# Kernel tuning notes

Hardware: AMD Instinct MI355X
Metric: run time of the kernel (lower is better)

Reference implementation:

```python
import jax, jax.numpy as jnp
import numpy as np
import math

WP, WF = 10, 10      # past/future window
EPS = 1e-8           # torch cosine_similarity eps
CLIP = 1.0 - 1e-6    # keep arccos (and its grad) finite
MAXN = 110           # hard-coded alpha width in the module


def setup_inputs() -> dict:
    key = jax.random.key(0)
    k1, k2, k3, k4, k5, k6 = jax.random.split(key, 6)
    B, L, G, N, D = 32, 110, 512, 40, 300
    node_features = jax.random.normal(k1, (B, L, G), jnp.float32)
    knowledge = jax.random.normal(k2, (B, L, N, D), jnp.float32)
    anew = jax.random.uniform(k3, (B, L, N), jnp.float32)
    var_sem = 2.0 / (G + G)
    var_con = 2.0 / (D + D)
    weight_sem = jax.random.normal(k4, (G, G), jnp.float32) * var_sem
    weight_con = jax.random.normal(k5, (D, D), jnp.float32) * var_con
    text_len = jax.random.randint(k6, (B,), 55, L + 1, jnp.int32)
    return dict(node_features=node_features, knowledge=knowledge, anew=anew,
                weight_sem=weight_sem, weight_con=weight_con, text_len=text_len)


def reference(node_features, knowledge, anew, weight_sem, weight_con, text_len):
    B, L, G = node_features.shape
    N = knowledge.shape[2]
    dt = node_features.dtype

    # window + validity mask, replaces per-(i,j) python slicing: [B, j, k]
    j = jnp.arange(L)[:, None]
    k = jnp.arange(L)[None, :]
    cur = text_len[:, None, None]
    mask = (k >= j - WP) & (k <= j + WF)
    mask = mask[None] & (k[None, :, :] <= cur - 1) & (j[None, :, :] < cur)
    fmask = mask.astype(dt)

    # ---- semantic branch: score = 1 - acos(cos_sim(f_j, W_sem f_k))/pi, windowed softmax
    att_sem = jnp.einsum('st,blt->bls', weight_sem, node_features)      # [B,L,G]
    num = jnp.einsum('bjg,bkg->bjk', node_features, att_sem)
    nf = jnp.maximum(jnp.linalg.norm(node_features, axis=-1), EPS)      # [B,L]
    na = jnp.maximum(jnp.linalg.norm(att_sem, axis=-1), EPS)            # [B,L]
    cos = num / (nf[:, :, None] * na[:, None, :])
    score = 1.0 - jnp.arccos(jnp.clip(cos, -CLIP, CLIP)) / math.pi
    neg = jnp.finfo(dt).min
    s = jnp.where(mask, score, neg)
    s = s - jnp.max(s, axis=-1, keepdims=True)
    e = jnp.exp(s) * fmask
    alphas_sem = e / jnp.maximum(jnp.sum(e, axis=-1, keepdims=True), EPS)  # [B,L,L]

    # ---- affinity transform of anew: v -> (||[v, v/2] - [0.5, 0]|| - 0.06467)/0.607468
    anew_aff = (jnp.sqrt((anew - 0.5) ** 2 + (0.5 * anew) ** 2) - 0.06467) / 0.607468

    # ---- contextual branch: windowed sum_n |cos_sim(aff_feat_{k,n}, knowledge_{j,n})|
    att_con = jnp.einsum('blns,st->blnt', knowledge, weight_con)        # [B,L,N,D]
    aff_feat = att_con * anew_aff[..., None]                            # [B,L,N,D]
    num_c = jnp.einsum('bknd,bjnd->bjkn', aff_feat, knowledge)          # [B,j,k,N]
    n_f = jnp.maximum(jnp.linalg.norm(aff_feat, axis=-1), EPS)          # [B,k,N]
    n_k = jnp.maximum(jnp.linalg.norm(knowledge, axis=-1), EPS)         # [B,j,N]
    cos_c = num_c / (n_f[:, None, :, :] * n_k[:, :, None, :])
    alphas_con = 10.0 * jnp.sum(jnp.abs(cos_c), axis=-1) * fmask        # [B,j,k]

    out = 0.5 * alphas_sem + 0.5 * alphas_con                           # [B,L,L]
    if L < MAXN:  # module hard-codes width 110
        out = jnp.pad(out, ((0, 0), (0, 0), (0, MAXN - L)))
    return out
```

## Files before the change

kernel.cpp:

```cpp
#include <hip/hip_runtime.h>
#include <hip/hip_bf16.h>
#include <math.h>

constexpr int Bb   = 32;
constexpr int Ls   = 110;
constexpr int Gs   = 512;
constexpr int Ns   = 40;
constexpr int Ds   = 300;
constexpr int WPc  = 10;
constexpr int WFc  = 10;
constexpr int MAXNc = 110;
constexpr float EPSf  = 1e-8f;
constexpr float CLIPf = 1.0f - 1e-6f;
constexpr int BL = Bb * Ls;
constexpr int Mrows = BL * Ns;
constexpr int BPITCH = 328;
constexpr int KST = 320;
constexpr int RGRP = Mrows / 256;

typedef __attribute__((ext_vector_type(8))) short short8_t;
typedef __attribute__((ext_vector_type(4))) short short4_t;
typedef __attribute__((ext_vector_type(4))) float floatx4;

__device__ __forceinline__ unsigned short bf16r(float f) {
  unsigned u = __float_as_uint(f);
  u += 0x7fffu + ((u >> 16) & 1u);
  return (unsigned short)(u >> 16);
}

__device__ __forceinline__ unsigned pkbf(float lo, float hi) {
  unsigned a = __float_as_uint(lo), b = __float_as_uint(hi);
  a += 0x7fffu + ((a >> 16) & 1u);
  b += 0x7fffu + ((b >> 16) & 1u);
  return (a >> 16) | (b & 0xffff0000u);
}

__device__ __forceinline__ short8_t cvt8(const float4 v0, const float4 v1) {
  union { short8_t s; unsigned u[4]; } p;
  p.u[0] = pkbf(v0.x, v0.y);
  p.u[1] = pkbf(v0.z, v0.w);
  p.u[2] = pkbf(v1.x, v1.y);
  p.u[3] = pkbf(v1.z, v1.w);
  return p.s;
}

__global__ __launch_bounds__(256) void transpose_wsem(const float* __restrict__ w,
                                                      float* __restrict__ wt) {
  __shared__ float tile[32][33];
  const int bx = blockIdx.x * 32;
  const int by = blockIdx.y * 32;
  const int tx = threadIdx.x;
  const int ty = threadIdx.y;
#pragma unroll
  for (int r = ty; r < 32; r += 8)
    tile[r][tx] = w[(by + r) * Gs + (bx + tx)];
  __syncthreads();
#pragma unroll
  for (int r = ty; r < 32; r += 8)
    wt[(bx + r) * Gs + (by + tx)] = tile[tx][r];
}

__global__ __launch_bounds__(256) void wct_prep(const float* __restrict__ wc,
                                                short* __restrict__ wct) {
  __shared__ float tile[32][33];
  const int t0 = blockIdx.x * 32;
  const int s0 = blockIdx.y * 32;
  const int tx = threadIdx.x, ty = threadIdx.y;
#pragma unroll
  for (int r = ty; r < 32; r += 8) {
    const int s = s0 + r, t = t0 + tx;
    tile[r][tx] = (s < Ds && t < Ds) ? wc[s * Ds + t] : 0.f;
  }
  __syncthreads();
#pragma unroll
  for (int r = ty; r < 32; r += 8) {
    const int t = t0 + r, s = s0 + tx;
    wct[t * KST + s] = (short)bf16r(tile[tx][r]);
  }
}

__global__ __launch_bounds__(256) void kn_prep(const float* __restrict__ kn,
                                               unsigned short* __restrict__ knb,
                                               float* __restrict__ kninv) {
  const int wid = (blockIdx.x * 256 + threadIdx.x) >> 6;
  const int lane = threadIdx.x & 63;
  const int nwaves = gridDim.x * 4;
  for (int row = wid; row < Mrows; row += nwaves) {
    const float* __restrict__ src = kn + (size_t)row * Ds;
    float4 v0 = make_float4(0.f, 0.f, 0.f, 0.f);
    float4 v1 = v0;
    const int d0 = lane * 8;
    if (lane < 37) {
      v0 = *reinterpret_cast<const float4*>(src + d0);
      v1 = *reinterpret_cast<const float4*>(src + d0 + 4);
    } else if (lane == 37) {
      v0 = *reinterpret_cast<const float4*>(src + d0);
    }
    float ss = v0.x * v0.x + v0.y * v0.y + v0.z * v0.z + v0.w * v0.w +
               v1.x * v1.x + v1.y * v1.y + v1.z * v1.z + v1.w * v1.w;
#pragma unroll
    for (int off = 32; off > 0; off >>= 1) ss += __shfl_xor(ss, off);
    if (lane < 40)
      *reinterpret_cast<short8_t*>(knb + (size_t)row * KST + d0) = cvt8(v0, v1);
    if (lane == 0) kninv[row] = 1.0f / fmaxf(sqrtf(ss), EPSf);
  }
}

__global__ __launch_bounds__(512) void sem_gemm(const float* __restrict__ nf,
                                                const float* __restrict__ wt,
                                                float* __restrict__ att_sem,
                                                float* __restrict__ na_arr) {
  const int bl0 = blockIdx.x * 8;
  const int s = threadIdx.x;
  const float* __restrict__ x0 = nf + (size_t)bl0 * Gs;
  float acc[8];
#pragma unroll
  for (int r = 0; r < 8; ++r) acc[r] = 0.f;
#pragma unroll 4
  for (int t = 0; t < Gs; ++t) {
    const float wv = wt[t * Gs + s];
#pragma unroll
    for (int r = 0; r < 8; ++r) acc[r] = fmaf(wv, x0[r * Gs + t], acc[r]);
  }
#pragma unroll
  for (int r = 0; r < 8; ++r) att_sem[(size_t)(bl0 + r) * Gs + s] = acc[r];

  __shared__ float partial[8][8];
  const int wave = s >> 6, lane = s & 63;
#pragma unroll
  for (int r = 0; r < 8; ++r) {
    float v = acc[r] * acc[r];
#pragma unroll
    for (int off = 32; off > 0; off >>= 1) v += __shfl_xor(v, off);
    if (lane == 0) partial[r][wave] = v;
  }
  __syncthreads();
  if (s < 8) {
    float sum = 0.f;
#pragma unroll
    for (int w2 = 0; w2 < 8; ++w2) sum += partial[s][w2];
    na_arr[bl0 + s] = fmaxf(sqrtf(sum), EPSf);
  }
}

__global__ __launch_bounds__(256) void sem_attn(const float* __restrict__ nf,
                                                const float* __restrict__ att_sem,
                                                const float* __restrict__ na_arr,
                                                const int* __restrict__ tlen,
                                                float* __restrict__ out) {
  const int blk = blockIdx.x;
  const int b = blk / Ls, j = blk % Ls;
  const int len = tlen[b];
  float* __restrict__ orow = out + (size_t)(b * Ls + j) * MAXNc;
  if (j >= len) {
    for (int k = threadIdx.x; k < MAXNc; k += 256) orow[k] = 0.f;
    return;
  }
  const int k0 = max(j - WPc, 0);
  const int k1 = min(j + WFc, len - 1);
  const int nk = k1 - k0 + 1;

  __shared__ float xs[Gs];
  __shared__ float sc[21];
  __shared__ float red[4];

  const float* __restrict__ x = nf + (size_t)(b * Ls + j) * Gs;
  float ss = 0.f;
  for (int t = threadIdx.x; t < Gs; t += 256) {
    const float v = x[t];
    xs[t] = v;
    ss += v * v;
  }
  const int wave = threadIdx.x >> 6, lane = threadIdx.x & 63;
#pragma unroll
  for (int off = 32; off > 0; off >>= 1) ss += __shfl_xor(ss, off);
  if (lane == 0) red[wave] = ss;
  __syncthreads();
  const float nfn = fmaxf(sqrtf(red[0] + red[1] + red[2] + red[3]), EPSf);

  for (int i = wave; i < nk; i += 4) {
    const int k = k0 + i;
    const float* __restrict__ as = att_sem + (size_t)(b * Ls + k) * Gs;
    float d = 0.f;
#pragma unroll
    for (int t = lane; t < Gs; t += 64) d = fmaf(xs[t], as[t], d);
#pragma unroll
    for (int off = 32; off > 0; off >>= 1) d += __shfl_xor(d, off);
    if (lane == 0) {
      float cs = d / (nfn * na_arr[b * Ls + k]);
      cs = fminf(fmaxf(cs, -CLIPf), CLIPf);
      sc[i] = 1.0f - acosf(cs) * (float)(1.0 / M_PI);
    }
  }
  __syncthreads();
  if (threadIdx.x == 0) {
    float m = -1e30f;
    for (int i = 0; i < nk; ++i) m = fmaxf(m, sc[i]);
    red[0] = m;
  }
  __syncthreads();
  const float m = red[0];
  if ((int)threadIdx.x < nk) sc[threadIdx.x] = expf(sc[threadIdx.x] - m);
  __syncthreads();
  if (threadIdx.x == 0) {
    float s = 0.f;
    for (int i = 0; i < nk; ++i) s += sc[i];
    red[1] = 1.0f / fmaxf(s, EPSf);
  }
  __syncthreads();
  const float inv = red[1];
  for (int k = threadIdx.x; k < MAXNc; k += 256) {
    float v = 0.f;
    if (k >= k0 && k <= k1) v = 0.5f * sc[k - k0] * inv;
    orow[k] = v;
  }
}

__global__ __launch_bounds__(256, 3) void con_gemm_mfma(const unsigned short* __restrict__ knb,
                                                        const short* __restrict__ wct,
                                                        const int* __restrict__ tlen,
                                                        unsigned short* __restrict__ ybar,
                                                        float* __restrict__ rowss) {
  const int lin = blockIdx.x;
  const int xcd = lin & 7, slot = lin >> 3;
  const int m = slot & 3;
  const int g = xcd + 8 * (slot >> 2);
  if (g >= RGRP) return;
  const int rowbase = g * 256;
  const int n0 = m * 80;

  __shared__ short Bl[80 * BPITCH];
  const int tid = threadIdx.x;
  for (int s = tid; s < 80 * 40; s += 256) {
    const int nl = s / 40, sl = s % 40;
    *reinterpret_cast<short8_t*>(&Bl[nl * BPITCH + sl * 8]) =
        *reinterpret_cast<const short8_t*>(wct + (n0 + nl) * KST + sl * 8);
  }
  __syncthreads();

  const int wave = tid >> 6, lane = tid & 63;
  const int quad = lane >> 4, l16 = lane & 15;
  const int wrow = rowbase + wave * 64;

  {
    bool any = false;
    for (int bl = wrow / Ns; bl <= (wrow + 63) / Ns; ++bl)
      any |= (bl % Ls) < tlen[bl / Ls];
    if (!any) return;
  }

  const unsigned short* arow[4];
#pragma unroll
  for (int tt = 0; tt < 4; ++tt)
    arow[tt] = knb + (size_t)(wrow + tt * 16 + l16) * KST + quad * 8;

  floatx4 acc[4][5];
#pragma unroll
  for (int tt = 0; tt < 4; ++tt)
#pragma unroll
    for (int i = 0; i < 5; ++i) acc[tt][i] = (floatx4){0.f, 0.f, 0.f, 0.f};

  short8_t A[3][4];
#pragma unroll
  for (int tt = 0; tt < 4; ++tt) {
    A[0][tt] = *reinterpret_cast<const short8_t*>(arow[tt]);
    A[1][tt] = *reinterpret_cast<const short8_t*>(arow[tt] + 32);
  }

#pragma unroll
  for (int c = 0; c < 10; ++c) {
    if (c < 8) {
#pragma unroll
      for (int tt = 0; tt < 4; ++tt)
        A[(c + 2) % 3][tt] =
            *reinterpret_cast<const short8_t*>(arow[tt] + (c + 2) * 32);
    }
#pragma unroll
    for (int i = 0; i < 5; ++i) {
      const short8_t bfrag = *reinterpret_cast<const short8_t*>(
          &Bl[(i * 16 + l16) * BPITCH + c * 32 + quad * 8]);
#pragma unroll
      for (int tt = 0; tt < 4; ++tt)
        acc[tt][i] = __builtin_amdgcn_mfma_f32_16x16x32_bf16(A[c % 3][tt], bfrag,
                                                             acc[tt][i], 0, 0, 0);
    }
  }

#pragma unroll
  for (int tt = 0; tt < 4; ++tt) {
    const int row0 = wrow + tt * 16;
    const int blA = row0 / Ns, blB = (row0 + 15) / Ns;
    const bool alive = ((blA % Ls) < tlen[blA / Ls]) | ((blB % Ls) < tlen[blB / Ls]);
    if (!alive) continue;
#pragma unroll
    for (int r = 0; r < 4; ++r) {
      float p = 0.f;
#pragma unroll
      for (int i = 0; i < 5; ++i) p = fmaf(acc[tt][i][r], acc[tt][i][r], p);
      p += __shfl_xor(p, 1);
      p += __shfl_xor(p, 2);
      p += __shfl_xor(p, 4);
      p += __shfl_xor(p, 8);
      if (l16 == 0) atomicAdd(&rowss[row0 + quad * 4 + r], p);
    }
#pragma unroll
    for (int i = 0; i < 5; ++i) {
      const int col = n0 + i * 16 + l16;
#pragma unroll
      for (int r = 0; r < 4; ++r)
        ybar[(size_t)(row0 + quad * 4 + r) * KST + col] = bf16r(acc[tt][i][r]);
    }
  }
}

__global__ __launch_bounds__(512) void con_attn_mfma(const unsigned short* __restrict__ knb,
                                                     const unsigned short* __restrict__ ybar,
                                                     const float* __restrict__ rowss,
                                                     const float* __restrict__ kninv,
                                                     const float* __restrict__ anew,
                                                     const int* __restrict__ tlen,
                                                     float* __restrict__ out) {
  const int b = blockIdx.x / 7;
  const int jt = blockIdx.x % 7;
  const int j0 = jt * 16;
  const int len = tlen[b];
  if (j0 >= len) return;
  const int kbase = min(max(j0 - WPc, 0), Ls - 48);

  const int tid = threadIdx.x;
  const int wave = tid >> 6, lane = tid & 63;
  const int quad = lane >> 4, l16 = lane & 15;

  __shared__ float red[8][768];

  const int jj = min(j0 + l16, Ls - 1);
  const size_t blj = (size_t)(b * Ls + jj);

  float outacc[3][4];
#pragma unroll
  for (int t = 0; t < 3; ++t)
#pragma unroll
    for (int r = 0; r < 4; ++r) outacc[t][r] = 0.f;

  const unsigned short* yrow[3];
  int krow_m[3];
#pragma unroll
  for (int t = 0; t < 3; ++t) {
    const int k = kbase + t * 16 + l16;
    yrow[t] = ybar + (size_t)(b * Ls + k) * Ns * KST;
    krow_m[t] = (b * Ls + k) * Ns;
  }

  for (int ni = 0; ni < 5; ++ni) {
    const int n = wave + ni * 8;
    const unsigned short* __restrict__ arow =
        knb + ((blj * Ns + n) * (size_t)KST) + quad * 8;

    float w_t[3];
#pragma unroll
    for (int t = 0; t < 3; ++t) {
      const int mm = krow_m[t] + n;
      const float a = anew[mm];
      const float ssqk = rowss[mm];
      const float aff = (sqrtf((a - 0.5f) * (a - 0.5f) + 0.25f * a * a) - 0.06467f) *
                        (1.0f / 0.607468f);
      w_t[t] = aff / fmaxf(aff * sqrtf(ssqk), EPSf);
    }
    const float kinv = kninv[blj * Ns + n];

    floatx4 S[3];
#pragma unroll
    for (int t = 0; t < 3; ++t) S[t] = (floatx4){0.f, 0.f, 0.f, 0.f};

#pragma unroll
    for (int c = 0; c < 10; ++c) {
      const short8_t afrag = *reinterpret_cast<const short8_t*>(arow + c * 32);
#pragma unroll
      for (int t = 0; t < 3; ++t) {
        const short8_t bfrag = *reinterpret_cast<const short8_t*>(
            yrow[t] + (size_t)n * KST + c * 32 + quad * 8);
        S[t] = __builtin_amdgcn_mfma_f32_16x16x32_bf16(afrag, bfrag, S[t], 0, 0, 0);
      }
    }

#pragma unroll
    for (int r = 0; r < 4; ++r) {
      const float kv = __shfl(kinv, quad * 4 + r);
#pragma unroll
      for (int t = 0; t < 3; ++t)
        outacc[t][r] = fmaf(kv * w_t[t], fabsf(S[t][r]), outacc[t][r]);
    }
  }

#pragma unroll
  for (int t = 0; t < 3; ++t)
#pragma unroll
    for (int r = 0; r < 4; ++r)
      red[wave][(quad * 4 + r) * 48 + t * 16 + l16] = outacc[t][r];
  __syncthreads();

  for (int idx = tid; idx < 768; idx += 512) {
    float s = 0.f;
#pragma unroll
    for (int w = 0; w < 8; ++w) s += red[w][idx];
    const int j = j0 + idx / 48;
    const int k = kbase + idx % 48;
    if (j < len && k < len && k >= j - WPc && k <= j + WFc)
      out[(size_t)(b * Ls + j) * MAXNc + k] += 5.0f * s;
  }
}

extern "C" void kernel_launch(void* const* d_in, const int* in_sizes, int n_in,
                              void* d_out, int out_size, void* d_ws, size_t ws_size,
                              hipStream_t stream) {
  const float* nf   = (const float*)d_in[0];
  const float* kn   = (const float*)d_in[1];
  const float* anew = (const float*)d_in[2];
  const float* wsem = (const float*)d_in[3];
  const float* wcon = (const float*)d_in[4];
  const int*   tlen = (const int*)d_in[5];
  float* out = (float*)d_out;

  float* att_sem = (float*)d_ws;
  float* na_arr  = att_sem + (size_t)BL * Gs;
  float* wt      = na_arr + BL;
  short* wct     = (short*)(wt + (size_t)Gs * Gs);
  float* rowss   = (float*)(wct + KST * KST);
  float* kninv   = rowss + Mrows;
  unsigned short* knb  = (unsigned short*)(kninv + Mrows);
  unsigned short* ybar = knb + (size_t)Mrows * KST;

  hipMemsetAsync(rowss, 0, (size_t)Mrows * sizeof(float), stream);
  transpose_wsem<<<dim3(16, 16), dim3(32, 8), 0, stream>>>(wsem, wt);
  wct_prep<<<dim3(10, 10), dim3(32, 8), 0, stream>>>(wcon, wct);
  kn_prep<<<2048, 256, 0, stream>>>(kn, knb, kninv);
  sem_gemm<<<BL / 8, 512, 0, stream>>>(nf, wt, att_sem, na_arr);
  sem_attn<<<BL, 256, 0, stream>>>(nf, att_sem, na_arr, tlen, out);
  con_gemm_mfma<<<2208, 256, 0, stream>>>(knb, wct, tlen, ybar, rowss);
  con_attn_mfma<<<Bb * 7, 512, 0, stream>>>(knb, ybar, rowss, kninv, anew, tlen, out);
}
```

Baseline: 482.7 us.

## Fuse knowledge bf16 conversion and norm into GEMM and attention kernels

Result: slower. 783.8 us (+62.4%).

```diff
diff --git a/kernel.cpp b/kernel.cpp
--- a/kernel.cpp
+++ b/kernel.cpp
@@ -79,33 +79,6 @@
   }
 }
 
-__global__ __launch_bounds__(256) void kn_prep(const float* __restrict__ kn,
-                                               unsigned short* __restrict__ knb,
-                                               float* __restrict__ kninv) {
-  const int wid = (blockIdx.x * 256 + threadIdx.x) >> 6;
-  const int lane = threadIdx.x & 63;
-  const int nwaves = gridDim.x * 4;
-  for (int row = wid; row < Mrows; row += nwaves) {
-    const float* __restrict__ src = kn + (size_t)row * Ds;
-    float4 v0 = make_float4(0.f, 0.f, 0.f, 0.f);
-    float4 v1 = v0;
-    const int d0 = lane * 8;
-    if (lane < 37) {
-      v0 = *reinterpret_cast<const float4*>(src + d0);
-      v1 = *reinterpret_cast<const float4*>(src + d0 + 4);
-    } else if (lane == 37) {
-      v0 = *reinterpret_cast<const float4*>(src + d0);
-    }
-    float ss = v0.x * v0.x + v0.y * v0.y + v0.z * v0.z + v0.w * v0.w +
-               v1.x * v1.x + v1.y * v1.y + v1.z * v1.z + v1.w * v1.w;
-#pragma unroll
-    for (int off = 32; off > 0; off >>= 1) ss += __shfl_xor(ss, off);
-    if (lane < 40)
-      *reinterpret_cast<short8_t*>(knb + (size_t)row * KST + d0) = cvt8(v0, v1);
-    if (lane == 0) kninv[row] = 1.0f / fmaxf(sqrtf(ss), EPSf);
-  }
-}
-
 __global__ __launch_bounds__(512) void sem_gemm(const float* __restrict__ nf,
                                                 const float* __restrict__ wt,
                                                 float* __restrict__ att_sem,
@@ -216,11 +189,12 @@
   }
 }
 
-__global__ __launch_bounds__(256, 3) void con_gemm_mfma(const unsigned short* __restrict__ knb,
+__global__ __launch_bounds__(256, 3) void con_gemm_mfma(const float* __restrict__ kn,
                                                         const short* __restrict__ wct,
                                                         const int* __restrict__ tlen,
                                                         unsigned short* __restrict__ ybar,
-                                                        float* __restrict__ rowss) {
+                                                        float* __restrict__ rowss,
+                                                        float* __restrict__ kninv) {
   const int lin = blockIdx.x;
   const int xcd = lin & 7, slot = lin >> 3;
   const int m = slot & 3;
@@ -249,10 +223,10 @@
     if (!any) return;
   }
 
-  const unsigned short* arow[4];
+  const float* arow[4];
 #pragma unroll
   for (int tt = 0; tt < 4; ++tt)
-    arow[tt] = knb + (size_t)(wrow + tt * 16 + l16) * KST + quad * 8;
+    arow[tt] = kn + (size_t)(wrow + tt * 16 + l16) * Ds + quad * 8;
 
   floatx4 acc[4][5];
 #pragma unroll
@@ -260,20 +234,46 @@
 #pragma unroll
     for (int i = 0; i < 5; ++i) acc[tt][i] = (floatx4){0.f, 0.f, 0.f, 0.f};
 
-  short8_t A[3][4];
+  float ssq[4] = {0.f, 0.f, 0.f, 0.f};
+
+  float4 F0[4], F1[4];
 #pragma unroll
   for (int tt = 0; tt < 4; ++tt) {
-    A[0][tt] = *reinterpret_cast<const short8_t*>(arow[tt]);
-    A[1][tt] = *reinterpret_cast<const short8_t*>(arow[tt] + 32);
+    F0[tt] = *reinterpret_cast<const float4*>(arow[tt]);
+    F1[tt] = *reinterpret_cast<const float4*>(arow[tt] + 4);
   }
 
 #pragma unroll
   for (int c = 0; c < 10; ++c) {
+    short8_t Af[4];
+#pragma unroll
+    for (int tt = 0; tt < 4; ++tt) {
+      ssq[tt] += F0[tt].x * F0[tt].x + F0[tt].y * F0[tt].y +
+                 F0[tt].z * F0[tt].z + F0[tt].w * F0[tt].w +
+                 F1[tt].x * F1[tt].x + F1[tt].y * F1[tt].y +
+                 F1[tt].z * F1[tt].z + F1[tt].w * F1[tt].w;
+      Af[tt] = cvt8(F0[tt], F1[tt]);
+    }
     if (c < 8) {
 #pragma unroll
-      for (int tt = 0; tt < 4; ++tt)
-        A[(c + 2) % 3][tt] =
-            *reinterpret_cast<const short8_t*>(arow[tt] + (c + 2) * 32);
+      for (int tt = 0; tt < 4; ++tt) {
+        F0[tt] = *reinterpret_cast<const float4*>(arow[tt] + (c + 1) * 32);
+        F1[tt] = *reinterpret_cast<const float4*>(arow[tt] + (c + 1) * 32 + 4);
+      }
+    } else if (c == 8) {
+#pragma unroll
+      for (int tt = 0; tt < 4; ++tt) {
+        float4 v0 = make_float4(0.f, 0.f, 0.f, 0.f);
+        float4 v1 = make_float4(0.f, 0.f, 0.f, 0.f);
+        if (quad == 0) {
+          v0 = *reinterpret_cast<const float4*>(arow[tt] + 288);
+          v1 = *reinterpret_cast<const float4*>(arow[tt] + 292);
+        } else if (quad == 1) {
+          v0 = *reinterpret_cast<const float4*>(arow[tt] + 288);
+        }
+        F0[tt] = v0;
+        F1[tt] = v1;
+      }
     }
 #pragma unroll
     for (int i = 0; i < 5; ++i) {
@@ -281,7 +281,7 @@
           &Bl[(i * 16 + l16) * BPITCH + c * 32 + quad * 8]);
 #pragma unroll
       for (int tt = 0; tt < 4; ++tt)
-        acc[tt][i] = __builtin_amdgcn_mfma_f32_16x16x32_bf16(A[c % 3][tt], bfrag,
+        acc[tt][i] = __builtin_amdgcn_mfma_f32_16x16x32_bf16(Af[tt], bfrag,
                                                              acc[tt][i], 0, 0, 0);
     }
   }
@@ -292,6 +292,13 @@
     const int blA = row0 / Ns, blB = (row0 + 15) / Ns;
     const bool alive = ((blA % Ls) < tlen[blA / Ls]) | ((blB % Ls) < tlen[blB / Ls]);
     if (!alive) continue;
+
+    float sq = ssq[tt];
+    sq += __shfl_xor(sq, 16);
+    sq += __shfl_xor(sq, 32);
+    if (lane < 16)
+      kninv[row0 + lane] = 1.0f / fmaxf(sqrtf(sq), EPSf);
+
 #pragma unroll
     for (int r = 0; r < 4; ++r) {
       float p = 0.f;
@@ -313,15 +320,17 @@
   }
 }
 
-__global__ __launch_bounds__(512) void con_attn_mfma(const unsigned short* __restrict__ knb,
+__global__ __launch_bounds__(512) void con_attn_mfma(const float* __restrict__ kn,
                                                      const unsigned short* __restrict__ ybar,
                                                      const float* __restrict__ rowss,
                                                      const float* __restrict__ kninv,
                                                      const float* __restrict__ anew,
                                                      const int* __restrict__ tlen,
                                                      float* __restrict__ out) {
-  const int b = blockIdx.x / 7;
-  const int jt = blockIdx.x % 7;
+  const int lin = blockIdx.x;
+  const int xcd = lin & 7, slot = lin >> 3;
+  const int b = xcd * 4 + slot / 7;
+  const int jt = slot % 7;
   const int j0 = jt * 16;
   const int len = tlen[b];
   if (j0 >= len) return;
@@ -353,8 +362,7 @@
 
   for (int ni = 0; ni < 5; ++ni) {
     const int n = wave + ni * 8;
-    const unsigned short* __restrict__ arow =
-        knb + ((blj * Ns + n) * (size_t)KST) + quad * 8;
+    const float* __restrict__ arow = kn + (blj * Ns + n) * (size_t)Ds + quad * 8;
 
     float w_t[3];
 #pragma unroll
@@ -374,7 +382,20 @@
 
 #pragma unroll
     for (int c = 0; c < 10; ++c) {
-      const short8_t afrag = *reinterpret_cast<const short8_t*>(arow + c * 32);
+      float4 v0 = make_float4(0.f, 0.f, 0.f, 0.f);
+      float4 v1 = make_float4(0.f, 0.f, 0.f, 0.f);
+      if (c < 9) {
+        v0 = *reinterpret_cast<const float4*>(arow + c * 32);
+        v1 = *reinterpret_cast<const float4*>(arow + c * 32 + 4);
+      } else {
+        if (quad == 0) {
+          v0 = *reinterpret_cast<const float4*>(arow + 288);
+          v1 = *reinterpret_cast<const float4*>(arow + 292);
+        } else if (quad == 1) {
+          v0 = *reinterpret_cast<const float4*>(arow + 288);
+        }
+      }
+      const short8_t afrag = cvt8(v0, v1);
 #pragma unroll
       for (int t = 0; t < 3; ++t) {
         const short8_t bfrag = *reinterpret_cast<const short8_t*>(
@@ -427,15 +448,13 @@
   short* wct     = (short*)(wt + (size_t)Gs * Gs);
   float* rowss   = (float*)(wct + KST * KST);
   float* kninv   = rowss + Mrows;
-  unsigned short* knb  = (unsigned short*)(kninv + Mrows);
-  unsigned short* ybar = knb + (size_t)Mrows * KST;
+  unsigned short* ybar = (unsigned short*)(kninv + Mrows);
 
   hipMemsetAsync(rowss, 0, (size_t)Mrows * sizeof(float), stream);
   transpose_wsem<<<dim3(16, 16), dim3(32, 8), 0, stream>>>(wsem, wt);
   wct_prep<<<dim3(10, 10), dim3(32, 8), 0, stream>>>(wcon, wct);
-  kn_prep<<<2048, 256, 0, stream>>>(kn, knb, kninv);
   sem_gemm<<<BL / 8, 512, 0, stream>>>(nf, wt, att_sem, na_arr);
   sem_attn<<<BL, 256, 0, stream>>>(nf, att_sem, na_arr, tlen, out);
-  con_gemm_mfma<<<2208, 256, 0, stream>>>(knb, wct, tlen, ybar, rowss);
-  con_attn_mfma<<<Bb * 7, 512, 0, stream>>>(knb, ybar, rowss, kninv, anew, tlen, out);
-}
+  con_gemm_mfma<<<2208, 256, 0, stream>>>(kn, wct, tlen, ybar, rowss, kninv);
+  con_attn_mfma<<<Bb * 7, 512, 0, stream>>>(kn, ybar, rowss, kninv, anew, tlen, out);
+}
```

## Pre-swizzle W_con into MFMA fragment order and read B directly from global

Applied to the files above, without the earlier changes.

New measurement: 502.8 us. 1.04x slower.

```diff
diff --git a/kernel.cpp b/kernel.cpp
--- a/kernel.cpp
+++ b/kernel.cpp
@@ -14,7 +14,6 @@
 constexpr float CLIPf = 1.0f - 1e-6f;
 constexpr int BL = Bb * Ls;
 constexpr int Mrows = BL * Ns;
-constexpr int BPITCH = 328;
 constexpr int KST = 320;
 constexpr int RGRP = Mrows / 256;
 
@@ -60,23 +59,21 @@
     wt[(bx + r) * Gs + (by + tx)] = tile[tx][r];
 }
 
-__global__ __launch_bounds__(256) void wct_prep(const float* __restrict__ wc,
-                                                short* __restrict__ wct) {
-  __shared__ float tile[32][33];
-  const int t0 = blockIdx.x * 32;
-  const int s0 = blockIdx.y * 32;
-  const int tx = threadIdx.x, ty = threadIdx.y;
-#pragma unroll
-  for (int r = ty; r < 32; r += 8) {
-    const int s = s0 + r, t = t0 + tx;
-    tile[r][tx] = (s < Ds && t < Ds) ? wc[s * Ds + t] : 0.f;
-  }
-  __syncthreads();
-#pragma unroll
-  for (int r = ty; r < 32; r += 8) {
-    const int t = t0 + r, s = s0 + tx;
-    wct[t * KST + s] = (short)bf16r(tile[tx][r]);
-  }
+__global__ __launch_bounds__(64) void wctf_prep(const float* __restrict__ wc,
+                                                short* __restrict__ wctf) {
+  const int fid = blockIdx.x;
+  const int nb = fid / 10, c = fid % 10;
+  const int lane = threadIdx.x;
+  const int t = nb * 16 + (lane & 15);
+  const int s0 = c * 32 + (lane >> 4) * 8;
+  short8_t v;
+#pragma unroll
+  for (int e = 0; e < 8; ++e) {
+    const int s = s0 + e;
+    const float f = (s < Ds && t < Ds) ? wc[s * Ds + t] : 0.f;
+    v[e] = (short)bf16r(f);
+  }
+  *reinterpret_cast<short8_t*>(wctf + ((size_t)fid * 64 + lane) * 8) = v;
 }
 
 __global__ __launch_bounds__(256) void kn_prep(const float* __restrict__ kn,
@@ -217,7 +214,7 @@
 }
 
 __global__ __launch_bounds__(256, 3) void con_gemm_mfma(const unsigned short* __restrict__ knb,
-                                                        const short* __restrict__ wct,
+                                                        const short* __restrict__ wctf,
                                                         const int* __restrict__ tlen,
                                                         unsigned short* __restrict__ ybar,
                                                         float* __restrict__ rowss) {
@@ -229,15 +226,7 @@
   const int rowbase = g * 256;
   const int n0 = m * 80;
 
-  __shared__ short Bl[80 * BPITCH];
   const int tid = threadIdx.x;
-  for (int s = tid; s < 80 * 40; s += 256) {
-    const int nl = s / 40, sl = s % 40;
-    *reinterpret_cast<short8_t*>(&Bl[nl * BPITCH + sl * 8]) =
-        *reinterpret_cast<const short8_t*>(wct + (n0 + nl) * KST + sl * 8);
-  }
-  __syncthreads();
-
   const int wave = tid >> 6, lane = tid & 63;
   const int quad = lane >> 4, l16 = lane & 15;
   const int wrow = rowbase + wave * 64;
@@ -249,6 +238,8 @@
     if (!any) return;
   }
 
+  const short* __restrict__ bbase = wctf + (size_t)(m * 5) * 5120;
+
   const unsigned short* arow[4];
 #pragma unroll
   for (int tt = 0; tt < 4; ++tt)
@@ -260,30 +251,30 @@
 #pragma unroll
     for (int i = 0; i < 5; ++i) acc[tt][i] = (floatx4){0.f, 0.f, 0.f, 0.f};
 
-  short8_t A[3][4];
-#pragma unroll
-  for (int tt = 0; tt < 4; ++tt) {
+  short8_t A[2][4];
+#pragma unroll
+  for (int tt = 0; tt < 4; ++tt)
     A[0][tt] = *reinterpret_cast<const short8_t*>(arow[tt]);
-    A[1][tt] = *reinterpret_cast<const short8_t*>(arow[tt] + 32);
-  }
 
 #pragma unroll
   for (int c = 0; c < 10; ++c) {
-    if (c < 8) {
+    short8_t bfr[5];
+#pragma unroll
+    for (int i = 0; i < 5; ++i)
+      bfr[i] = *reinterpret_cast<const short8_t*>(
+          bbase + ((size_t)(i * 10 + c) * 64 + lane) * 8);
+    if (c < 9) {
 #pragma unroll
       for (int tt = 0; tt < 4; ++tt)
-        A[(c + 2) % 3][tt] =
-            *reinterpret_cast<const short8_t*>(arow[tt] + (c + 2) * 32);
-    }
-#pragma unroll
-    for (int i = 0; i < 5; ++i) {
-      const short8_t bfrag = *reinterpret_cast<const short8_t*>(
-          &Bl[(i * 16 + l16) * BPITCH + c * 32 + quad * 8]);
+        A[(c + 1) & 1][tt] =
+            *reinterpret_cast<const short8_t*>(arow[tt] + (c + 1) * 32);
+    }
+#pragma unroll
+    for (int i = 0; i < 5; ++i)
 #pragma unroll
       for (int tt = 0; tt < 4; ++tt)
-        acc[tt][i] = __builtin_amdgcn_mfma_f32_16x16x32_bf16(A[c % 3][tt], bfrag,
+        acc[tt][i] = __builtin_amdgcn_mfma_f32_16x16x32_bf16(A[c & 1][tt], bfr[i],
                                                              acc[tt][i], 0, 0, 0);
-    }
   }
 
 #pragma unroll
@@ -292,6 +283,7 @@
     const int blA = row0 / Ns, blB = (row0 + 15) / Ns;
     const bool alive = ((blA % Ls) < tlen[blA / Ls]) | ((blB % Ls) < tlen[blB / Ls]);
     if (!alive) continue;
+
 #pragma unroll
     for (int r = 0; r < 4; ++r) {
       float p = 0.f;
@@ -320,8 +312,10 @@
                                                      const float* __restrict__ anew,
                                                      const int* __restrict__ tlen,
                                                      float* __restrict__ out) {
-  const int b = blockIdx.x / 7;
-  const int jt = blockIdx.x % 7;
+  const int lin = blockIdx.x;
+  const int xcd = lin & 7, slot = lin >> 3;
+  const int b = xcd * 4 + slot / 7;
+  const int jt = slot % 7;
   const int j0 = jt * 16;
   const int len = tlen[b];
   if (j0 >= len) return;
@@ -424,18 +418,18 @@
   float* att_sem = (float*)d_ws;
   float* na_arr  = att_sem + (size_t)BL * Gs;
   float* wt      = na_arr + BL;
-  short* wct     = (short*)(wt + (size_t)Gs * Gs);
-  float* rowss   = (float*)(wct + KST * KST);
+  short* wctf    = (short*)(wt + (size_t)Gs * Gs);
+  float* rowss   = (float*)(wctf + 200 * 64 * 8);
   float* kninv   = rowss + Mrows;
   unsigned short* knb  = (unsigned short*)(kninv + Mrows);
   unsigned short* ybar = knb + (size_t)Mrows * KST;
 
   hipMemsetAsync(rowss, 0, (size_t)Mrows * sizeof(float), stream);
   transpose_wsem<<<dim3(16, 16), dim3(32, 8), 0, stream>>>(wsem, wt);
-  wct_prep<<<dim3(10, 10), dim3(32, 8), 0, stream>>>(wcon, wct);
+  wctf_prep<<<200, 64, 0, stream>>>(wcon, wctf);
   kn_prep<<<2048, 256, 0, stream>>>(kn, knb, kninv);
   sem_gemm<<<BL / 8, 512, 0, stream>>>(nf, wt, att_sem, na_arr);
   sem_attn<<<BL, 256, 0, stream>>>(nf, att_sem, na_arr, tlen, out);
-  con_gemm_mfma<<<2208, 256, 0, stream>>>(knb, wct, tlen, ybar, rowss);
+  con_gemm_mfma<<<2208, 256, 0, stream>>>(knb, wctf, tlen, ybar, rowss);
   con_attn_mfma<<<Bb * 7, 512, 0, stream>>>(knb, ybar, rowss, kninv, anew, tlen, out);
 }
```

## Merge independent kernels into two block-partitioned launches for concurrency

Applied to the files above, without the earlier changes.

New measurement: 501.1 us. 1.04x slower.

```diff
diff --git a/kernel.cpp b/kernel.cpp
--- a/kernel.cpp
+++ b/kernel.cpp
@@ -18,8 +18,11 @@
 constexpr int KST = 320;
 constexpr int RGRP = Mrows / 256;
 
+constexpr int PREP_BLOCKS = 2048;
+constexpr int SGEMM_BLOCKS = BL / 8;
+constexpr int CGEMM_BLOCKS = 2208;
+
 typedef __attribute__((ext_vector_type(8))) short short8_t;
-typedef __attribute__((ext_vector_type(4))) short short4_t;
 typedef __attribute__((ext_vector_type(4))) float floatx4;
 
 __device__ __forceinline__ unsigned short bf16r(float f) {
@@ -79,236 +82,235 @@
   }
 }
 
-__global__ __launch_bounds__(256) void kn_prep(const float* __restrict__ kn,
-                                               unsigned short* __restrict__ knb,
-                                               float* __restrict__ kninv) {
-  const int wid = (blockIdx.x * 256 + threadIdx.x) >> 6;
-  const int lane = threadIdx.x & 63;
-  const int nwaves = gridDim.x * 4;
-  for (int row = wid; row < Mrows; row += nwaves) {
-    const float* __restrict__ src = kn + (size_t)row * Ds;
-    float4 v0 = make_float4(0.f, 0.f, 0.f, 0.f);
-    float4 v1 = v0;
-    const int d0 = lane * 8;
-    if (lane < 37) {
-      v0 = *reinterpret_cast<const float4*>(src + d0);
-      v1 = *reinterpret_cast<const float4*>(src + d0 + 4);
-    } else if (lane == 37) {
-      v0 = *reinterpret_cast<const float4*>(src + d0);
-    }
-    float ss = v0.x * v0.x + v0.y * v0.y + v0.z * v0.z + v0.w * v0.w +
-               v1.x * v1.x + v1.y * v1.y + v1.z * v1.z + v1.w * v1.w;
+__global__ __launch_bounds__(512) void fused_prep_semgemm(
+    const float* __restrict__ kn, unsigned short* __restrict__ knb,
+    float* __restrict__ kninv,
+    const float* __restrict__ nf, const float* __restrict__ wt,
+    float* __restrict__ att_sem, float* __restrict__ na_arr) {
+  __shared__ float partial[8][8];
+
+  if (blockIdx.x < PREP_BLOCKS) {
+    const int wid = (blockIdx.x * 512 + threadIdx.x) >> 6;
+    const int lane = threadIdx.x & 63;
+    const int nwaves = PREP_BLOCKS * 8;
+    for (int row = wid; row < Mrows; row += nwaves) {
+      const float* __restrict__ src = kn + (size_t)row * Ds;
+      float4 v0 = make_float4(0.f, 0.f, 0.f, 0.f);
+      float4 v1 = v0;
+      const int d0 = lane * 8;
+      if (lane < 37) {
+        v0 = *reinterpret_cast<const float4*>(src + d0);
+        v1 = *reinterpret_cast<const float4*>(src + d0 + 4);
+      } else if (lane == 37) {
+        v0 = *reinterpret_cast<const float4*>(src + d0);
+      }
+      float ss = v0.x * v0.x + v0.y * v0.y + v0.z * v0.z + v0.w * v0.w +
+                 v1.x * v1.x + v1.y * v1.y + v1.z * v1.z + v1.w * v1.w;
+#pragma unroll
+      for (int off = 32; off > 0; off >>= 1) ss += __shfl_xor(ss, off);
+      if (lane < 40)
+        *reinterpret_cast<short8_t*>(knb + (size_t)row * KST + d0) = cvt8(v0, v1);
+      if (lane == 0) kninv[row] = 1.0f / fmaxf(sqrtf(ss), EPSf);
+    }
+  } else {
+    const int bl0 = (blockIdx.x - PREP_BLOCKS) * 8;
+    const int s = threadIdx.x;
+    const float* __restrict__ x0 = nf + (size_t)bl0 * Gs;
+    float acc[8];
+#pragma unroll
+    for (int r = 0; r < 8; ++r) acc[r] = 0.f;
+#pragma unroll 4
+    for (int t = 0; t < Gs; ++t) {
+      const float wv = wt[t * Gs + s];
+#pragma unroll
+      for (int r = 0; r < 8; ++r) acc[r] = fmaf(wv, x0[r * Gs + t], acc[r]);
+    }
+#pragma unroll
+    for (int r = 0; r < 8; ++r) att_sem[(size_t)(bl0 + r) * Gs + s] = acc[r];
+
+    const int wave = s >> 6, lane = s & 63;
+#pragma unroll
+    for (int r = 0; r < 8; ++r) {
+      float v = acc[r] * acc[r];
+#pragma unroll
+      for (int off = 32; off > 0; off >>= 1) v += __shfl_xor(v, off);
+      if (lane == 0) partial[r][wave] = v;
+    }
+    __syncthreads();
+    if (s < 8) {
+      float sum = 0.f;
+#pragma unroll
+      for (int w2 = 0; w2 < 8; ++w2) sum += partial[s][w2];
+      na_arr[bl0 + s] = fmaxf(sqrtf(sum), EPSf);
+    }
+  }
+}
+
+__global__ __launch_bounds__(256, 3) void fused_congemm_semattn(
+    const unsigned short* __restrict__ knb, const short* __restrict__ wct,
+    const int* __restrict__ tlen,
+    unsigned short* __restrict__ ybar, float* __restrict__ rowss,
+    const float* __restrict__ nf, const float* __restrict__ att_sem,
+    const float* __restrict__ na_arr, float* __restrict__ out) {
+  __shared__ short Bl[80 * BPITCH];
+  __shared__ float sred[4];
+  __shared__ float ssc[21];
+
+  if (blockIdx.x < CGEMM_BLOCKS) {
+    const int lin = blockIdx.x;
+    const int xcd = lin & 7, slot = lin >> 3;
+    const int m = slot & 3;
+    const int g = xcd + 8 * (slot >> 2);
+    if (g >= RGRP) return;
+    const int rowbase = g * 256;
+    const int n0 = m * 80;
+
+    const int tid = threadIdx.x;
+    for (int s = tid; s < 80 * 40; s += 256) {
+      const int nl = s / 40, sl = s % 40;
+      *reinterpret_cast<short8_t*>(&Bl[nl * BPITCH + sl * 8]) =
+          *reinterpret_cast<const short8_t*>(wct + (n0 + nl) * KST + sl * 8);
+    }
+    __syncthreads();
+
+    const int wave = tid >> 6, lane = tid & 63;
+    const int quad = lane >> 4, l16 = lane & 15;
+    const int wrow = rowbase + wave * 64;
+
+    {
+      bool any = false;
+      for (int bl = wrow / Ns; bl <= (wrow + 63) / Ns; ++bl)
+        any |= (bl % Ls) < tlen[bl / Ls];
+      if (!any) return;
+    }
+
+    const unsigned short* arow[4];
+#pragma unroll
+    for (int tt = 0; tt < 4; ++tt)
+      arow[tt] = knb + (size_t)(wrow + tt * 16 + l16) * KST + quad * 8;
+
+    floatx4 acc[4][5];
+#pragma unroll
+    for (int tt = 0; tt < 4; ++tt)
+#pragma unroll
+      for (int i = 0; i < 5; ++i) acc[tt][i] = (floatx4){0.f, 0.f, 0.f, 0.f};
+
+    short8_t A[3][4];
+#pragma unroll
+    for (int tt = 0; tt < 4; ++tt) {
+      A[0][tt] = *reinterpret_cast<const short8_t*>(arow[tt]);
+      A[1][tt] = *reinterpret_cast<const short8_t*>(arow[tt] + 32);
+    }
+
+#pragma unroll
+    for (int c = 0; c < 10; ++c) {
+      if (c < 8) {
+#pragma unroll
+        for (int tt = 0; tt < 4; ++tt)
+          A[(c + 2) % 3][tt] =
+              *reinterpret_cast<const short8_t*>(arow[tt] + (c + 2) * 32);
+      }
+#pragma unroll
+      for (int i = 0; i < 5; ++i) {
+        const short8_t bfrag = *reinterpret_cast<const short8_t*>(
+            &Bl[(i * 16 + l16) * BPITCH + c * 32 + quad * 8]);
+#pragma unroll
+        for (int tt = 0; tt < 4; ++tt)
+          acc[tt][i] = __builtin_amdgcn_mfma_f32_16x16x32_bf16(
+              A[c % 3][tt], bfrag, acc[tt][i], 0, 0, 0);
+      }
+    }
+
+#pragma unroll
+    for (int tt = 0; tt < 4; ++tt) {
+      const int row0 = wrow + tt * 16;
+      const int blA = row0 / Ns, blB = (row0 + 15) / Ns;
+      const bool alive =
+          ((blA % Ls) < tlen[blA / Ls]) | ((blB % Ls) < tlen[blB / Ls]);
+      if (!alive) continue;
+
+#pragma unroll
+      for (int r = 0; r < 4; ++r) {
+        float p = 0.f;
+#pragma unroll
+        for (int i = 0; i < 5; ++i) p = fmaf(acc[tt][i][r], acc[tt][i][r], p);
+        p += __shfl_xor(p, 1);
+        p += __shfl_xor(p, 2);
+        p += __shfl_xor(p, 4);
+        p += __shfl_xor(p, 8);
+        if (l16 == 0) atomicAdd(&rowss[row0 + quad * 4 + r], p);
+      }
+#pragma unroll
+      for (int i = 0; i < 5; ++i) {
+        const int col = n0 + i * 16 + l16;
+#pragma unroll
+        for (int r = 0; r < 4; ++r)
+          ybar[(size_t)(row0 + quad * 4 + r) * KST + col] = bf16r(acc[tt][i][r]);
+      }
+    }
+  } else {
+    float* xs = reinterpret_cast<float*>(Bl);
+    const int blk = blockIdx.x - CGEMM_BLOCKS;
+    const int b = blk / Ls, j = blk % Ls;
+    const int len = tlen[b];
+    float* __restrict__ orow = out + (size_t)(b * Ls + j) * MAXNc;
+    if (j >= len) {
+      for (int k = threadIdx.x; k < MAXNc; k += 256) orow[k] = 0.f;
+      return;
+    }
+    const int k0 = max(j - WPc, 0);
+    const int k1 = min(j + WFc, len - 1);
+    const int nk = k1 - k0 + 1;
+
+    const float* __restrict__ x = nf + (size_t)(b * Ls + j) * Gs;
+    float ss = 0.f;
+    for (int t = threadIdx.x; t < Gs; t += 256) {
+      const float v = x[t];
+      xs[t] = v;
+      ss += v * v;
+    }
+    const int wave = threadIdx.x >> 6, lane = threadIdx.x & 63;
 #pragma unroll
     for (int off = 32; off > 0; off >>= 1) ss += __shfl_xor(ss, off);
-    if (lane < 40)
-      *reinterpret_cast<short8_t*>(knb + (size_t)row * KST + d0) = cvt8(v0, v1);
-    if (lane == 0) kninv[row] = 1.0f / fmaxf(sqrtf(ss), EPSf);
-  }
-}
-
-__global__ __launch_bounds__(512) void sem_gemm(const float* __restrict__ nf,
-                                                const float* __restrict__ wt,
-                                                float* __restrict__ att_sem,
-                                                float* __restrict__ na_arr) {
-  const int bl0 = blockIdx.x * 8;
-  const int s = threadIdx.x;
-  const float* __restrict__ x0 = nf + (size_t)bl0 * Gs;
-  float acc[8];
-#pragma unroll
-  for (int r = 0; r < 8; ++r) acc[r] = 0.f;
-#pragma unroll 4
-  for (int t = 0; t < Gs; ++t) {
-    const float wv = wt[t * Gs + s];
-#pragma unroll
-    for (int r = 0; r < 8; ++r) acc[r] = fmaf(wv, x0[r * Gs + t], acc[r]);
-  }
-#pragma unroll
-  for (int r = 0; r < 8; ++r) att_sem[(size_t)(bl0 + r) * Gs + s] = acc[r];
-
-  __shared__ float partial[8][8];
-  const int wave = s >> 6, lane = s & 63;
-#pragma unroll
-  for (int r = 0; r < 8; ++r) {
-    float v = acc[r] * acc[r];
-#pragma unroll
-    for (int off = 32; off > 0; off >>= 1) v += __shfl_xor(v, off);
-    if (lane == 0) partial[r][wave] = v;
-  }
-  __syncthreads();
-  if (s < 8) {
-    float sum = 0.f;
-#pragma unroll
-    for (int w2 = 0; w2 < 8; ++w2) sum += partial[s][w2];
-    na_arr[bl0 + s] = fmaxf(sqrtf(sum), EPSf);
-  }
-}
-
-__global__ __launch_bounds__(256) void sem_attn(const float* __restrict__ nf,
-                                                const float* __restrict__ att_sem,
-                                                const float* __restrict__ na_arr,
-                                                const int* __restrict__ tlen,
-                                                float* __restrict__ out) {
-  const int blk = blockIdx.x;
-  const int b = blk / Ls, j = blk % Ls;
-  const int len = tlen[b];
-  float* __restrict__ orow = out + (size_t)(b * Ls + j) * MAXNc;
-  if (j >= len) {
-    for (int k = threadIdx.x; k < MAXNc; k += 256) orow[k] = 0.f;
-    return;
-  }
-  const int k0 = max(j - WPc, 0);
-  const int k1 = min(j + WFc, len - 1);
-  const int nk = k1 - k0 + 1;
-
-  __shared__ float xs[Gs];
-  __shared__ float sc[21];
-  __shared__ float red[4];
-
-  const float* __restrict__ x = nf + (size_t)(b * Ls + j) * Gs;
-  float ss = 0.f;
-  for (int t = threadIdx.x; t < Gs; t += 256) {
-    const float v = x[t];
-    xs[t] = v;
-    ss += v * v;
-  }
-  const int wave = threadIdx.x >> 6, lane = threadIdx.x & 63;
-#pragma unroll
-  for (int off = 32; off > 0; off >>= 1) ss += __shfl_xor(ss, off);
-  if (lane == 0) red[wave] = ss;
-  __syncthreads();
-  const float nfn = fmaxf(sqrtf(red[0] + red[1] + red[2] + red[3]), EPSf);
-
-  for (int i = wave; i < nk; i += 4) {
-    const int k = k0 + i;
-    const float* __restrict__ as = att_sem + (size_t)(b * Ls + k) * Gs;
-    float d = 0.f;
-#pragma unroll
-    for (int t = lane; t < Gs; t += 64) d = fmaf(xs[t], as[t], d);
-#pragma unroll
-    for (int off = 32; off > 0; off >>= 1) d += __shfl_xor(d, off);
-    if (lane == 0) {
-      float cs = d / (nfn * na_arr[b * Ls + k]);
-      cs = fminf(fmaxf(cs, -CLIPf), CLIPf);
-      sc[i] = 1.0f - acosf(cs) * (float)(1.0 / M_PI);
-    }
-  }
-  __syncthreads();
-  if (threadIdx.x == 0) {
-    float m = -1e30f;
-    for (int i = 0; i < nk; ++i) m = fmaxf(m, sc[i]);
-    red[0] = m;
-  }
-  __syncthreads();
-  const float m = red[0];
-  if ((int)threadIdx.x < nk) sc[threadIdx.x] = expf(sc[threadIdx.x] - m);
-  __syncthreads();
-  if (threadIdx.x == 0) {
-    float s = 0.f;
-    for (int i = 0; i < nk; ++i) s += sc[i];
-    red[1] = 1.0f / fmaxf(s, EPSf);
-  }
-  __syncthreads();
-  const float inv = red[1];
-  for (int k = threadIdx.x; k < MAXNc; k += 256) {
-    float v = 0.f;
-    if (k >= k0 && k <= k1) v = 0.5f * sc[k - k0] * inv;
-    orow[k] = v;
-  }
-}
-
-__global__ __launch_bounds__(256, 3) void con_gemm_mfma(const unsigned short* __restrict__ knb,
-                                                        const short* __restrict__ wct,
-                                                        const int* __restrict__ tlen,
-                                                        unsigned short* __restrict__ ybar,
-                                                        float* __restrict__ rowss) {
-  const int lin = blockIdx.x;
-  const int xcd = lin & 7, slot = lin >> 3;
-  const int m = slot & 3;
-  const int g = xcd + 8 * (slot >> 2);
-  if (g >= RGRP) return;
-  const int rowbase = g * 256;
-  const int n0 = m * 80;
-
-  __shared__ short Bl[80 * BPITCH];
-  const int tid = threadIdx.x;
-  for (int s = tid; s < 80 * 40; s += 256) {
-    const int nl = s / 40, sl = s % 40;
-    *reinterpret_cast<short8_t*>(&Bl[nl * BPITCH + sl * 8]) =
-        *reinterpret_cast<const short8_t*>(wct + (n0 + nl) * KST + sl * 8);
-  }
-  __syncthreads();
-
-  const int wave = tid >> 6, lane = tid & 63;
-  const int quad = lane >> 4, l16 = lane & 15;
-  const int wrow = rowbase + wave * 64;
-
-  {
-    bool any = false;
-    for (int bl = wrow / Ns; bl <= (wrow + 63) / Ns; ++bl)
-      any |= (bl % Ls) < tlen[bl / Ls];
-    if (!any) return;
-  }
-
-  const unsigned short* arow[4];
-#pragma unroll
-  for (int tt = 0; tt < 4; ++tt)
-    arow[tt] = knb + (size_t)(wrow + tt * 16 + l16) * KST + quad * 8;
-
-  floatx4 acc[4][5];
-#pragma unroll
-  for (int tt = 0; tt < 4; ++tt)
-#pragma unroll
-    for (int i = 0; i < 5; ++i) acc[tt][i] = (floatx4){0.f, 0.f, 0.f, 0.f};
-
-  short8_t A[3][4];
-#pragma unroll
-  for (int tt = 0; tt < 4; ++tt) {
-    A[0][tt] = *reinterpret_cast<const short8_t*>(arow[tt]);
-    A[1][tt] = *reinterpret_cast<const short8_t*>(arow[tt] + 32);
-  }
-
-#pragma unroll
-  for (int c = 0; c < 10; ++c) {
-    if (c < 8) {
-#pragma unroll
-      for (int tt = 0; tt < 4; ++tt)
-        A[(c + 2) % 3][tt] =
-            *reinterpret_cast<const short8_t*>(arow[tt] + (c + 2) * 32);
-    }
-#pragma unroll
-    for (int i = 0; i < 5; ++i) {
-      const short8_t bfrag = *reinterpret_cast<const short8_t*>(
-          &Bl[(i * 16 + l16) * BPITCH + c * 32 + quad * 8]);
-#pragma unroll
-      for (int tt = 0; tt < 4; ++tt)
-        acc[tt][i] = __builtin_amdgcn_mfma_f32_16x16x32_bf16(A[c % 3][tt], bfrag,
-                                                             acc[tt][i], 0, 0, 0);
-    }
-  }
-
-#pragma unroll
-  for (int tt = 0; tt < 4; ++tt) {
-    const int row0 = wrow + tt * 16;
-    const int blA = row0 / Ns, blB = (row0 + 15) / Ns;
-    const bool alive = ((blA % Ls) < tlen[blA / Ls]) | ((blB % Ls) < tlen[blB / Ls]);
-    if (!alive) continue;
-#pragma unroll
-    for (int r = 0; r < 4; ++r) {
-      float p = 0.f;
-#pragma unroll
-      for (int i = 0; i < 5; ++i) p = fmaf(acc[tt][i][r], acc[tt][i][r], p);
-      p += __shfl_xor(p, 1);
-      p += __shfl_xor(p, 2);
-      p += __shfl_xor(p, 4);
-      p += __shfl_xor(p, 8);
-      if (l16 == 0) atomicAdd(&rowss[row0 + quad * 4 + r], p);
-    }
-#pragma unroll
-    for (int i = 0; i < 5; ++i) {
-      const int col = n0 + i * 16 + l16;
-#pragma unroll
-      for (int r = 0; r < 4; ++r)
-        ybar[(size_t)(row0 + quad * 4 + r) * KST + col] = bf16r(acc[tt][i][r]);
+    if (lane == 0) sred[wave] = ss;
+    __syncthreads();
+    const float nfn = fmaxf(sqrtf(sred[0] + sred[1] + sred[2] + sred[3]), EPSf);
+
+    for (int i = wave; i < nk; i += 4) {
+      const int k = k0 + i;
+      const float* __restrict__ as = att_sem + (size_t)(b * Ls + k) * Gs;
+      float d = 0.f;
+#pragma unroll
+      for (int t = lane; t < Gs; t += 64) d = fmaf(xs[t], as[t], d);
+#pragma unroll
+      for (int off = 32; off > 0; off >>= 1) d += __shfl_xor(d, off);
+      if (lane == 0) {
+        float cs = d / (nfn * na_arr[b * Ls + k]);
+        cs = fminf(fmaxf(cs, -CLIPf), CLIPf);
+        ssc[i] = 1.0f - acosf(cs) * (float)(1.0 / M_PI);
+      }
+    }
+    __syncthreads();
+    if (threadIdx.x == 0) {
+      float mx = -1e30f;
+      for (int i = 0; i < nk; ++i) mx = fmaxf(mx, ssc[i]);
+      sred[0] = mx;
+    }
+    __syncthreads();
+    const float mx = sred[0];
+    if ((int)threadIdx.x < nk) ssc[threadIdx.x] = expf(ssc[threadIdx.x] - mx);
+    __syncthreads();
+    if (threadIdx.x == 0) {
+      float s = 0.f;
+      for (int i = 0; i < nk; ++i) s += ssc[i];
+      sred[1] = 1.0f / fmaxf(s, EPSf);
+    }
+    __syncthreads();
+    const float inv = sred[1];
+    for (int k = threadIdx.x; k < MAXNc; k += 256) {
+      float v = 0.f;
+      if (k >= k0 && k <= k1) v = 0.5f * ssc[k - k0] * inv;
+      orow[k] = v;
     }
   }
 }
@@ -433,9 +435,9 @@
   hipMemsetAsync(rowss, 0, (size_t)Mrows * sizeof(float), stream);
   transpose_wsem<<<dim3(16, 16), dim3(32, 8), 0, stream>>>(wsem, wt);
   wct_prep<<<dim3(10, 10), dim3(32, 8), 0, stream>>>(wcon, wct);
-  kn_prep<<<2048, 256, 0, stream>>>(kn, knb, kninv);
-  sem_gemm<<<BL / 8, 512, 0, stream>>>(nf, wt, att_sem, na_arr);
-  sem_attn<<<BL, 256, 0, stream>>>(nf, att_sem, na_arr, tlen, out);
-  con_gemm_mfma<<<2208, 256, 0, stream>>>(knb, wct, tlen, ybar, rowss);
+  fused_prep_semgemm<<<PREP_BLOCKS + SGEMM_BLOCKS, 512, 0, stream>>>(
+      kn, knb, kninv, nf, wt, att_sem, na_arr);
+  fused_congemm_semattn<<<CGEMM_BLOCKS + BL, 256, 0, stream>>>(
+      knb, wct, tlen, ybar, rowss, nf, att_sem, na_arr, out);
   con_attn_mfma<<<Bb * 7, 512, 0, stream>>>(knb, ybar, rowss, kninv, anew, tlen, out);
 }
```
